# Optimization experiments

Measured on AMD Instinct MI355X. Metric: run time of the kernel, lower is better.

## Reference

```python
import jax, jax.numpy as jnp
from jax import lax
import numpy as np

N, C, D, KNN = 32768, 1000, 1024, 16
EPS_EUC = 1e-12
EPS_COS = 1e-8
COS_THRESH = 0.85


def setup_inputs() -> dict:
    key = jax.random.key(0)
    k1, k2, k3 = jax.random.split(key, 3)
    feature = jax.random.normal(k1, (N, D), dtype=jnp.float32)
    pred = jax.random.normal(k2, (N, C), dtype=jnp.float32)
    unlabeled_index = jnp.arange(N, dtype=jnp.int64) if jax.config.jax_enable_x64 else jnp.arange(N, dtype=jnp.int32)
    # module state: centroids (from FeaturePool), top-N score buffer (init -1), fake index buffer (init -1)
    centroids = jax.random.normal(k3, (C, D), dtype=jnp.float32)
    pred_top_N = jnp.full((C, KNN), -1.0, dtype=jnp.float32)
    fake_index = jnp.full((C, KNN), -1, dtype=jnp.int32)
    return {"feature": feature, "pred": pred, "unlabeled_index": unlabeled_index,
            "centroids": centroids, "pred_top_N": pred_top_N, "fake_index": fake_index}


def reference(feature, pred, unlabeled_index, centroids, pred_top_N, fake_index):
    xx = jnp.sum(feature * feature, axis=1, keepdims=True)          # [N,1]
    yy = jnp.sum(centroids * centroids, axis=1)[None, :]            # [1,C]
    euc = jnp.sqrt(jnp.clip(xx + yy - 2.0 * (feature @ centroids.T), EPS_EUC, None))
    euc_id = jnp.argmin(euc, axis=1)                                # [N]

    scores = jnp.max(jax.nn.softmax(pred, axis=1), axis=1)          # [N] max softmax prob

    # cosine similarity of every sample to every centroid [N, C]
    f_n = feature / jnp.clip(jnp.linalg.norm(feature, axis=1, keepdims=True), EPS_COS, None)
    c_n = centroids / jnp.clip(jnp.linalg.norm(centroids, axis=1, keepdims=True), EPS_COS, None)
    cos = f_n @ c_n.T
    label_idx = jnp.argmax(cos, axis=1)                             # [N]
    cos_max = jnp.max(cos, axis=1)                                  # [N]

    # label[i] = label_idx if (cos-argmax == euc-argmin and cos_max > 0.85) else -1
    label = jnp.where((label_idx == euc_id) & (cos_max > COS_THRESH),
                      label_idx.astype(jnp.float32), -1.0)

    # sequential bounded top-N scatter update of (pred_top_N, fake_index)
    def step(carry, x):
        ptn, fidx = carry
        li, sc, ui = x
        row = ptn[li]                        # [KNN]
        mi = jnp.argmin(row)
        upd = sc > row[mi]
        ptn = ptn.at[li, mi].set(jnp.where(upd, sc, row[mi]))
        fidx = fidx.at[li, mi].set(jnp.where(upd, ui.astype(fidx.dtype), fidx[li, mi]))
        return (ptn, fidx), None

    (ptn_new, fidx_new), _ = lax.scan(step, (pred_top_N, fake_index),
                                      (label_idx, scores, unlabeled_index))
    return label, ptn_new, fidx_new
```

## Files before the change

kernel.cpp:

```cpp
#include <hip/hip_runtime.h>
#include <hip/hip_bf16.h>
#include <math.h>

#define NS 32768
#define NC 1000
#define CP 1024
#define DD 1024
#define KN 16

typedef __attribute__((ext_vector_type(8))) short bf16x8;
typedef __attribute__((ext_vector_type(4))) float f32x4;
typedef __attribute__((ext_vector_type(4))) float float4v;
typedef __attribute__((ext_vector_type(4))) int int4v;
typedef __attribute__((ext_vector_type(8))) unsigned short u16x8;
typedef __attribute__((ext_vector_type(4))) unsigned short u16x4;

__device__ __forceinline__ unsigned short f2bf(float f) {
  unsigned u = __float_as_uint(f);
  u += 0x7FFFu + ((u >> 16) & 1u);
  return (unsigned short)(u >> 16);
}
__device__ __forceinline__ float bf2f(unsigned short h) {
  return __uint_as_float(((unsigned)h) << 16);
}

#define GLL16(g, l) __builtin_amdgcn_global_load_lds( \
    (const __attribute__((address_space(1))) void*)(g), \
    (__attribute__((address_space(3))) void*)(l), 16, 0, 0)

__global__ __launch_bounds__(256) void k_cast_cent(
    const float* __restrict__ Cm, unsigned short* __restrict__ Cb,
    float* __restrict__ cnorm2, float* __restrict__ invc) {
  int c = blockIdx.x;
  int tid = threadIdx.x;
  float sq = 0.f;
  if (c < NC) {
    float4v v = ((const float4v*)(Cm + (size_t)c * DD))[tid];
    sq = v[0]*v[0] + v[1]*v[1] + v[2]*v[2] + v[3]*v[3];
    u16x4 o = { f2bf(v[0]), f2bf(v[1]), f2bf(v[2]), f2bf(v[3]) };
    *(u16x4*)(Cb + (size_t)c * DD + tid * 4) = o;
  } else {
    u16x4 z = { 0, 0, 0, 0 };
    *(u16x4*)(Cb + (size_t)c * DD + tid * 4) = z;
  }
  for (int off = 32; off; off >>= 1) sq += __shfl_xor(sq, off);
  __shared__ float red[4];
  int lane = tid & 63, wid = tid >> 6;
  if (!lane) red[wid] = sq;
  __syncthreads();
  if (!tid) {
    float s = red[0] + red[1] + red[2] + red[3];
    cnorm2[c] = s;
    float n = sqrtf(s); if (n < 1e-8f) n = 1e-8f;
    invc[c] = (c < NC) ? 1.0f / n : 0.0f;
  }
}

__global__ __launch_bounds__(256) void k_cast_feat(
    const float* __restrict__ A, unsigned short* __restrict__ Ab) {
  int t = blockIdx.x * 256 + threadIdx.x;
  const float4v* src = (const float4v*)A + (size_t)t * 2;
  float4v a = src[0], b = src[1];
  u16x8 o = { f2bf(a[0]), f2bf(a[1]), f2bf(a[2]), f2bf(a[3]),
              f2bf(b[0]), f2bf(b[1]), f2bf(b[2]), f2bf(b[3]) };
  *(u16x8*)(Ab + (size_t)t * 8) = o;
}

#define MF(a_, b_, c_) __builtin_amdgcn_mfma_f32_16x16x32_bf16(a_, b_, c_, 0, 0, 0)
#define RD(base_, i_) (*(const bf16x8*)((base_) + (i_) * 1024 + aoff))
#define SA(s_, b_) do { \
    GLL16(pA0 + (s_) * 32, ldsB + (b_) * 16384 + dA0); \
    GLL16(pA1 + (s_) * 32, ldsB + (b_) * 16384 + dA1); } while (0)
#define SB(s_, b_) do { \
    GLL16(pB0 + (s_) * 32, ldsB + 65536 + (b_) * 16384 + dA0); \
    GLL16(pB1 + (s_) * 32, ldsB + 65536 + (b_) * 16384 + dA1); } while (0)
#define VM4 asm volatile("s_waitcnt vmcnt(4)" ::: "memory")
#define VM0 asm volatile("s_waitcnt vmcnt(0)" ::: "memory")
#define MFMA4x4(M0) do { \
    acc[M0+0][0] = MF(af0, bv0, acc[M0+0][0]); \
    acc[M0+0][1] = MF(af0, bv1, acc[M0+0][1]); \
    acc[M0+0][2] = MF(af0, bv2, acc[M0+0][2]); \
    acc[M0+0][3] = MF(af0, bv3, acc[M0+0][3]); \
    acc[M0+1][0] = MF(af1, bv0, acc[M0+1][0]); \
    acc[M0+1][1] = MF(af1, bv1, acc[M0+1][1]); \
    acc[M0+1][2] = MF(af1, bv2, acc[M0+1][2]); \
    acc[M0+1][3] = MF(af1, bv3, acc[M0+1][3]); \
    acc[M0+2][0] = MF(af2, bv0, acc[M0+2][0]); \
    acc[M0+2][1] = MF(af2, bv1, acc[M0+2][1]); \
    acc[M0+2][2] = MF(af2, bv2, acc[M0+2][2]); \
    acc[M0+2][3] = MF(af2, bv3, acc[M0+2][3]); \
    acc[M0+3][0] = MF(af3, bv0, acc[M0+3][0]); \
    acc[M0+3][1] = MF(af3, bv1, acc[M0+3][1]); \
    acc[M0+3][2] = MF(af3, bv2, acc[M0+3][2]); \
    acc[M0+3][3] = MF(af3, bv3, acc[M0+3][3]); } while (0)
#define GSTEP(s_, STAGEA_, STAGEB_, GATE_) do { \
    const char* Ab_ = ldsB + ((s_) & 3) * 16384 + wrOff; \
    const char* Bb_ = ldsB + 65536 + ((s_) & 3) * 16384 + wcOff; \
    af0 = RD(Ab_, 0); af1 = RD(Ab_, 1); af2 = RD(Ab_, 2); af3 = RD(Ab_, 3); \
    bv0 = RD(Bb_, 0); bv1 = RD(Bb_, 1); bv2 = RD(Bb_, 2); bv3 = RD(Bb_, 3); \
    STAGEA_; \
    __builtin_amdgcn_s_barrier(); \
    __builtin_amdgcn_s_setprio(1); \
    MFMA4x4(0); \
    __builtin_amdgcn_s_setprio(0); \
    __builtin_amdgcn_s_barrier(); \
    af0 = RD(Ab_, 4); af1 = RD(Ab_, 5); af2 = RD(Ab_, 6); af3 = RD(Ab_, 7); \
    STAGEB_; \
    __builtin_amdgcn_s_barrier(); \
    __builtin_amdgcn_s_setprio(1); \
    MFMA4x4(4); \
    __builtin_amdgcn_s_setprio(0); \
    GATE_; \
    __builtin_amdgcn_s_barrier(); \
  } while (0)

__global__ __launch_bounds__(512, 1) void k_gemm(
    const unsigned short* __restrict__ A,
    const unsigned short* __restrict__ B,
    unsigned short* __restrict__ Dout) {
  __shared__ unsigned short lds[65536];
  char* ldsB = (char*)lds;
  int tid = threadIdx.x, lane = tid & 63, wid = tid >> 6;
  int wr = wid >> 2, wc = wid & 3;
  int bid = (blockIdx.x & 7) * 64 + (blockIdx.x >> 3);
  int cb = bid & 3, rb = bid >> 2;
  int brow = rb * 256, bcol = cb * 256;

  f32x4 acc[8][4];
#pragma unroll
  for (int m = 0; m < 8; ++m)
#pragma unroll
    for (int n = 0; n < 4; ++n) acc[m][n] = (f32x4){0.f, 0.f, 0.f, 0.f};

  int f0 = wid * 64 + lane, f1 = f0 + 512;
  int gl0 = (f0 & 3) ^ ((f0 >> 3) & 3);
  int gl1 = (f1 & 3) ^ ((f1 >> 3) & 3);
  const unsigned short* pA0 = A + (size_t)(brow + (f0 >> 2)) * DD + gl0 * 8;
  const unsigned short* pA1 = A + (size_t)(brow + (f1 >> 2)) * DD + gl1 * 8;
  const unsigned short* pB0 = B + (size_t)(bcol + (f0 >> 2)) * DD + gl0 * 8;
  const unsigned short* pB1 = B + (size_t)(bcol + (f1 >> 2)) * DD + gl1 * 8;
  int dA0 = f0 * 16, dA1 = f1 * 16;

  int aoff = (lane & 15) * 64 + (((lane >> 4) ^ ((lane >> 1) & 3)) * 16);
  int wrOff = wr * 8192;
  int wcOff = wc * 4096;

  bf16x8 af0, af1, af2, af3, bv0, bv1, bv2, bv3;

  SA(0, 0); SB(0, 0);
  SA(1, 1); SB(1, 1);
  VM4;
  __builtin_amdgcn_s_barrier();

  for (int s = 0; s < 30; ++s) {
    int bn = (s & 3) ^ 2;
    GSTEP(s, SA(s + 2, bn), SB(s + 2, bn), VM4);
  }
  GSTEP(30, (void)0, (void)0, VM0);
  GSTEP(31, (void)0, (void)0, (void)0);

  int colb = bcol + wc * 64 + (lane & 15);
  int rowb = brow + wr * 128 + ((lane >> 4) << 2);
#pragma unroll
  for (int m = 0; m < 8; ++m)
#pragma unroll
    for (int n = 0; n < 4; ++n)
#pragma unroll
      for (int j = 0; j < 4; ++j)
        Dout[(size_t)(rowb + m * 16 + j) * CP + colb + n * 16] = f2bf(acc[m][n][j]);
}

__global__ __launch_bounds__(256) void k_score(
    const float* __restrict__ P, float* __restrict__ scores) {
  int i = blockIdx.x, tid = threadIdx.x;
  const float* row = P + (size_t)i * NC;
  bool act = tid < 250;
  float p0 = 0, p1 = 0, p2 = 0, p3 = 0, mx = -1e30f;
  if (act) {
    int b = tid * 4;
    p0 = row[b]; p1 = row[b + 1]; p2 = row[b + 2]; p3 = row[b + 3];
    mx = fmaxf(fmaxf(p0, p1), fmaxf(p2, p3));
  }
  for (int off = 32; off; off >>= 1) mx = fmaxf(mx, __shfl_xor(mx, off));
  __shared__ float wmax[4];
  __shared__ double wsum[4];
  int lane = tid & 63, wid = tid >> 6;
  if (!lane) wmax[wid] = mx;
  __syncthreads();
  float m = fmaxf(fmaxf(wmax[0], wmax[1]), fmaxf(wmax[2], wmax[3]));
  double s = 0.0;
  if (act)
    s = (double)__expf(p0 - m) + (double)__expf(p1 - m) +
        (double)__expf(p2 - m) + (double)__expf(p3 - m);
  for (int off = 32; off; off >>= 1) s += __shfl_xor(s, off);
  if (!lane) wsum[wid] = s;
  __syncthreads();
  if (!tid) scores[i] = (float)(1.0 / (wsum[0] + wsum[1] + wsum[2] + wsum[3]));
}

__global__ __launch_bounds__(256) void k_argmax(
    const unsigned short* __restrict__ Dot, const float* __restrict__ invc,
    const float* __restrict__ cnorm2, const float* __restrict__ feat,
    const float* __restrict__ cent, float* __restrict__ label_out,
    int* __restrict__ lidx) {
  __shared__ float s_inv[CP], s_cn[CP];
  int tid = threadIdx.x;
#pragma unroll
  for (int q = 0; q < 4; ++q) {
    int c = q * 256 + tid;
    s_inv[c] = invc[c]; s_cn[c] = cnorm2[c];
  }
  __syncthreads();
  int lane = tid & 63, wid = tid >> 6;
  int i = blockIdx.x * 4 + wid;
  const unsigned short* drow = Dot + (size_t)i * CP;

  float v[16];
  float dmax = -1e30f; int darg = CP;
  float emin = 1e30f;  int earg = CP;
#pragma unroll
  for (int it = 0; it < 16; ++it) {
    int c = it * 64 + lane;
    float val, ev;
    if (c < NC) {
      float d = bf2f(drow[c]);
      val = d * s_inv[c];
      ev = s_cn[c] - 2.0f * d;
    } else { val = -1e30f; ev = 1e30f; }
    v[it] = val;
    if (val > dmax) { dmax = val; darg = c; }
    if (ev < emin)  { emin = ev;  earg = c; }
  }
  for (int off = 32; off; off >>= 1) {
    float om = __shfl_xor(dmax, off); int oi = __shfl_xor(darg, off);
    if (om > dmax || (om == dmax && oi < darg)) { dmax = om; darg = oi; }
    float oe = __shfl_xor(emin, off); int oj = __shfl_xor(earg, off);
    if (oe < emin || (oe == emin && oj < earg)) { emin = oe; earg = oj; }
  }
  const float MARGIN = 0.15f;
  unsigned long long cmask[16]; int ccnt = 0;
#pragma unroll
  for (int it = 0; it < 16; ++it) {
    int c = it * 64 + lane;
    bool cand = (c < NC) && (v[it] >= dmax - MARGIN);
    cmask[it] = __ballot(cand);
    ccnt += __popcll(cmask[it]);
  }
  int finalArg = darg;
  double cosmax_d = -2.0;
  bool need = (ccnt > 1) || (dmax > 10.0f);
  if (need) {
    float xv[16]; double sx = 0.0;
    const float* xr = feat + (size_t)i * DD;
#pragma unroll
    for (int t = 0; t < 16; ++t) {
      float x = xr[t * 64 + lane]; xv[t] = x; sx += (double)x * (double)x;
    }
    for (int off = 32; off; off >>= 1) sx += __shfl_xor(sx, off);
    double nx = sqrt(sx); if (nx < 1e-8) nx = 1e-8;
    double best = -2.0; int besti = CP;
    for (int it = 0; it < 16; ++it) {
      unsigned long long mk = cmask[it];
      while (mk) {
        int b = __builtin_ctzll(mk); mk &= mk - 1;
        int c = it * 64 + b;
        const float* cr = cent + (size_t)c * DD;
        double s = 0.0, s2 = 0.0;
#pragma unroll
        for (int t = 0; t < 16; ++t) {
          double cv = (double)cr[t * 64 + lane];
          s += (double)xv[t] * cv; s2 += cv * cv;
        }
        for (int off = 32; off; off >>= 1) {
          s += __shfl_xor(s, off); s2 += __shfl_xor(s2, off);
        }
        double nc = sqrt(s2); if (nc < 1e-8) nc = 1e-8;
        double cs = s / (nx * nc);
        if (cs > best) { best = cs; besti = c; }
      }
    }
    finalArg = besti; cosmax_d = best;
  }
  if (!lane) {
    lidx[i] = finalArg;
    float lab = -1.0f;
    if (need && finalArg == earg && cosmax_d > 0.85) lab = (float)finalArg;
    label_out[i] = lab;
  }
}

__global__ __launch_bounds__(64) void k_scan(
    const int* __restrict__ lidx, const float* __restrict__ scores,
    const int* __restrict__ uidx, const float* __restrict__ ptn_in,
    const int* __restrict__ fidx_in, float* __restrict__ out_ptn,
    float* __restrict__ out_fidx) {
  int c = blockIdx.x;
  int lane = threadIdx.x;
  float row[KN]; int idx[KN];
#pragma unroll
  for (int j = 0; j < KN; ++j) {
    row[j] = ptn_in[c * KN + j];
    idx[j] = fidx_in[c * KN + j];
  }
  for (int base = 0; base < NS; base += 256) {
    int l0 = lidx[base + lane];
    int l1 = lidx[base + 64 + lane];
    int l2 = lidx[base + 128 + lane];
    int l3 = lidx[base + 192 + lane];
#pragma unroll
    for (int q = 0; q < 4; ++q) {
      int lab = (q == 0) ? l0 : (q == 1) ? l1 : (q == 2) ? l2 : l3;
      unsigned long long m = __ballot(lab == c);
      while (m) {
        int b = __builtin_ctzll(m); m &= m - 1;
        int i = base + q * 64 + b;
        float s = scores[i];
        int ui = uidx[i];
        int mi = 0; float mn = row[0];
#pragma unroll
        for (int t = 1; t < KN; ++t)
          if (row[t] < mn) { mn = row[t]; mi = t; }
        if (s > mn) {
#pragma unroll
          for (int t = 0; t < KN; ++t)
            if (t == mi) { row[t] = s; idx[t] = ui; }
        }
      }
    }
  }
  if (!lane) {
#pragma unroll
    for (int j = 0; j < KN; ++j) {
      out_ptn[c * KN + j] = row[j];
      out_fidx[c * KN + j] = (float)idx[j];
    }
  }
}

extern "C" void kernel_launch(void* const* d_in, const int* in_sizes, int n_in,
                              void* d_out, int out_size, void* d_ws, size_t ws_size,
                              hipStream_t stream) {
  const float* feature = (const float*)d_in[0];
  const float* pred    = (const float*)d_in[1];
  const int*   uidx    = (const int*)d_in[2];
  const float* cent    = (const float*)d_in[3];
  const float* ptn_in  = (const float*)d_in[4];
  const int*   fidx_in = (const int*)d_in[5];
  float* out = (float*)d_out;

  char* ws = (char*)d_ws;
  unsigned short* cent_bf = (unsigned short*)(ws);
  unsigned short* feat_bf = (unsigned short*)(ws + (2ull << 20));
  unsigned short* dot_bf  = (unsigned short*)(ws + (66ull << 20));
  float* scores = (float*)(ws + (130ull << 20));
  int*   lidx   = (int*)  (ws + (130ull << 20) + (128ull << 10));
  float* cnorm2 = (float*)(ws + (130ull << 20) + (256ull << 10));
  float* invc   = (float*)(ws + (130ull << 20) + (260ull << 10));

  hipLaunchKernelGGL(k_cast_cent, dim3(CP), dim3(256), 0, stream,
                     cent, cent_bf, cnorm2, invc);
  hipLaunchKernelGGL(k_cast_feat, dim3((NS * DD / 8) / 256), dim3(256), 0, stream,
                     feature, feat_bf);
  hipLaunchKernelGGL(k_gemm, dim3((NS / 256) * (CP / 256)), dim3(512), 0, stream,
                     feat_bf, cent_bf, dot_bf);
  hipLaunchKernelGGL(k_score, dim3(NS), dim3(256), 0, stream, pred, scores);
  hipLaunchKernelGGL(k_argmax, dim3(NS / 4), dim3(256), 0, stream,
                     dot_bf, invc, cnorm2, feature, cent, out, lidx);
  hipLaunchKernelGGL(k_scan, dim3(NC), dim3(64), 0, stream,
                     lidx, scores, uidx, ptn_in, fidx_in,
                     out + NS, out + NS + NC * KN);
}
```

Before: 237.6 us.

## Fuse feature fp32-to-bf16 cast into GEMM A-tile loading

Removes the separate feature cast kernel and has the GEMM load fp32 feature rows directly into registers, convert them to bf16 and write them to LDS. The pipeline is restructured with ping-pong register buffers for A, async global-to-LDS loads kept only for B, and fewer barriers per k-step. This drops a 128MB fp32 read plus a 64MB bf16 write/read round trip. In exchange the GEMM now reads fp32 A from global once per column block (4x redundancy), and adds register pressure and VALU conversion work inside the MFMA loop.

Result: no change. 242.2 us (+2.0%).

```diff
diff --git a/kernel.cpp b/kernel.cpp
--- a/kernel.cpp
+++ b/kernel.cpp
@@ -56,26 +56,31 @@
   }
 }
 
-__global__ __launch_bounds__(256) void k_cast_feat(
-    const float* __restrict__ A, unsigned short* __restrict__ Ab) {
-  int t = blockIdx.x * 256 + threadIdx.x;
-  const float4v* src = (const float4v*)A + (size_t)t * 2;
-  float4v a = src[0], b = src[1];
-  u16x8 o = { f2bf(a[0]), f2bf(a[1]), f2bf(a[2]), f2bf(a[3]),
-              f2bf(b[0]), f2bf(b[1]), f2bf(b[2]), f2bf(b[3]) };
-  *(u16x8*)(Ab + (size_t)t * 8) = o;
-}
-
 #define MF(a_, b_, c_) __builtin_amdgcn_mfma_f32_16x16x32_bf16(a_, b_, c_, 0, 0, 0)
 #define RD(base_, i_) (*(const bf16x8*)((base_) + (i_) * 1024 + aoff))
-#define SA(s_, b_) do { \
-    GLL16(pA0 + (s_) * 32, ldsB + (b_) * 16384 + dA0); \
-    GLL16(pA1 + (s_) * 32, ldsB + (b_) * 16384 + dA1); } while (0)
-#define SB(s_, b_) do { \
-    GLL16(pB0 + (s_) * 32, ldsB + 65536 + (b_) * 16384 + dA0); \
-    GLL16(pB1 + (s_) * 32, ldsB + 65536 + (b_) * 16384 + dA1); } while (0)
-#define VM4 asm volatile("s_waitcnt vmcnt(4)" ::: "memory")
+#define LAE(s_) do { \
+    ea = ((const float4v*)(pA0 + (s_) * 32))[0]; \
+    eb = ((const float4v*)(pA0 + (s_) * 32))[1]; \
+    ec = ((const float4v*)(pA1 + (s_) * 32))[0]; \
+    ed = ((const float4v*)(pA1 + (s_) * 32))[1]; } while (0)
+#define LAO(s_) do { \
+    oa = ((const float4v*)(pA0 + (s_) * 32))[0]; \
+    ob = ((const float4v*)(pA0 + (s_) * 32))[1]; \
+    oc = ((const float4v*)(pA1 + (s_) * 32))[0]; \
+    od = ((const float4v*)(pA1 + (s_) * 32))[1]; } while (0)
+#define SB2(s_) do { \
+    GLL16(pB0 + (s_) * 32, ldsB + 65536 + ((s_) & 3) * 16384 + dA0); \
+    GLL16(pB1 + (s_) * 32, ldsB + 65536 + ((s_) & 3) * 16384 + dA1); } while (0)
+#define CVW(s_, va, vb, vc, vd) do { \
+    u16x8 w0 = { f2bf(va[0]), f2bf(va[1]), f2bf(va[2]), f2bf(va[3]), \
+                 f2bf(vb[0]), f2bf(vb[1]), f2bf(vb[2]), f2bf(vb[3]) }; \
+    u16x8 w1 = { f2bf(vc[0]), f2bf(vc[1]), f2bf(vc[2]), f2bf(vc[3]), \
+                 f2bf(vd[0]), f2bf(vd[1]), f2bf(vd[2]), f2bf(vd[3]) }; \
+    *(u16x8*)(ldsB + ((s_) & 3) * 16384 + dA0) = w0; \
+    *(u16x8*)(ldsB + ((s_) & 3) * 16384 + dA1) = w1; } while (0)
+#define VM6 asm volatile("s_waitcnt vmcnt(6)" ::: "memory")
 #define VM0 asm volatile("s_waitcnt vmcnt(0)" ::: "memory")
+#define LGKM0 asm volatile("s_waitcnt lgkmcnt(0)" ::: "memory")
 #define MFMA4x4(M0) do { \
     acc[M0+0][0] = MF(af0, bv0, acc[M0+0][0]); \
     acc[M0+0][1] = MF(af0, bv1, acc[M0+0][1]); \
@@ -93,29 +98,23 @@
     acc[M0+3][1] = MF(af3, bv1, acc[M0+3][1]); \
     acc[M0+3][2] = MF(af3, bv2, acc[M0+3][2]); \
     acc[M0+3][3] = MF(af3, bv3, acc[M0+3][3]); } while (0)
-#define GSTEP(s_, STAGEA_, STAGEB_, GATE_) do { \
+#define KSTEP(s_, ISSUE_, WBANK_, GATE_) do { \
     const char* Ab_ = ldsB + ((s_) & 3) * 16384 + wrOff; \
     const char* Bb_ = ldsB + 65536 + ((s_) & 3) * 16384 + wcOff; \
     af0 = RD(Ab_, 0); af1 = RD(Ab_, 1); af2 = RD(Ab_, 2); af3 = RD(Ab_, 3); \
     bv0 = RD(Bb_, 0); bv1 = RD(Bb_, 1); bv2 = RD(Bb_, 2); bv3 = RD(Bb_, 3); \
-    STAGEA_; \
-    __builtin_amdgcn_s_barrier(); \
-    __builtin_amdgcn_s_setprio(1); \
-    MFMA4x4(0); \
-    __builtin_amdgcn_s_setprio(0); \
-    __builtin_amdgcn_s_barrier(); \
+    ISSUE_; \
+    __builtin_amdgcn_s_setprio(1); MFMA4x4(0); __builtin_amdgcn_s_setprio(0); \
     af0 = RD(Ab_, 4); af1 = RD(Ab_, 5); af2 = RD(Ab_, 6); af3 = RD(Ab_, 7); \
-    STAGEB_; \
-    __builtin_amdgcn_s_barrier(); \
-    __builtin_amdgcn_s_setprio(1); \
-    MFMA4x4(4); \
-    __builtin_amdgcn_s_setprio(0); \
+    WBANK_; \
+    __builtin_amdgcn_s_setprio(1); MFMA4x4(4); __builtin_amdgcn_s_setprio(0); \
+    LGKM0; \
     GATE_; \
     __builtin_amdgcn_s_barrier(); \
   } while (0)
 
 __global__ __launch_bounds__(512, 1) void k_gemm(
-    const unsigned short* __restrict__ A,
+    const float* __restrict__ Af,
     const unsigned short* __restrict__ B,
     unsigned short* __restrict__ Dout) {
   __shared__ unsigned short lds[65536];
@@ -135,8 +134,8 @@
   int f0 = wid * 64 + lane, f1 = f0 + 512;
   int gl0 = (f0 & 3) ^ ((f0 >> 3) & 3);
   int gl1 = (f1 & 3) ^ ((f1 >> 3) & 3);
-  const unsigned short* pA0 = A + (size_t)(brow + (f0 >> 2)) * DD + gl0 * 8;
-  const unsigned short* pA1 = A + (size_t)(brow + (f1 >> 2)) * DD + gl1 * 8;
+  const float* pA0 = Af + (size_t)(brow + (f0 >> 2)) * DD + gl0 * 8;
+  const float* pA1 = Af + (size_t)(brow + (f1 >> 2)) * DD + gl1 * 8;
   const unsigned short* pB0 = B + (size_t)(bcol + (f0 >> 2)) * DD + gl0 * 8;
   const unsigned short* pB1 = B + (size_t)(bcol + (f1 >> 2)) * DD + gl1 * 8;
   int dA0 = f0 * 16, dA1 = f1 * 16;
@@ -146,18 +145,21 @@
   int wcOff = wc * 4096;
 
   bf16x8 af0, af1, af2, af3, bv0, bv1, bv2, bv3;
-
-  SA(0, 0); SB(0, 0);
-  SA(1, 1); SB(1, 1);
-  VM4;
+  float4v ea, eb, ec, ed, oa, ob, oc, od;
+
+  LAE(0); SB2(0);
+  LAO(1); SB2(1);
+  CVW(0, ea, eb, ec, ed);
+  LGKM0;
+  VM6;
   __builtin_amdgcn_s_barrier();
 
-  for (int s = 0; s < 30; ++s) {
-    int bn = (s & 3) ^ 2;
-    GSTEP(s, SA(s + 2, bn), SB(s + 2, bn), VM4);
-  }
-  GSTEP(30, (void)0, (void)0, VM0);
-  GSTEP(31, (void)0, (void)0, (void)0);
+  for (int s = 0; s < 30; s += 2) {
+    KSTEP(s,     { LAE(s + 2); SB2(s + 2); }, CVW(s + 1, oa, ob, oc, od), VM6);
+    KSTEP(s + 1, { LAO(s + 3); SB2(s + 3); }, CVW(s + 2, ea, eb, ec, ed), VM6);
+  }
+  KSTEP(30, (void)0, CVW(31, oa, ob, oc, od), VM0);
+  KSTEP(31, (void)0, (void)0, (void)0);
 
   int colb = bcol + wc * 64 + (lane & 15);
   int rowb = brow + wr * 128 + ((lane >> 4) << 2);
@@ -350,7 +352,6 @@
 
   char* ws = (char*)d_ws;
   unsigned short* cent_bf = (unsigned short*)(ws);
-  unsigned short* feat_bf = (unsigned short*)(ws + (2ull << 20));
   unsigned short* dot_bf  = (unsigned short*)(ws + (66ull << 20));
   float* scores = (float*)(ws + (130ull << 20));
   int*   lidx   = (int*)  (ws + (130ull << 20) + (128ull << 10));
@@ -359,10 +360,8 @@
 
   hipLaunchKernelGGL(k_cast_cent, dim3(CP), dim3(256), 0, stream,
                      cent, cent_bf, cnorm2, invc);
-  hipLaunchKernelGGL(k_cast_feat, dim3((NS * DD / 8) / 256), dim3(256), 0, stream,
-                     feature, feat_bf);
   hipLaunchKernelGGL(k_gemm, dim3((NS / 256) * (CP / 256)), dim3(512), 0, stream,
-                     feat_bf, cent_bf, dot_bf);
+                     feature, cent_bf, dot_bf);
   hipLaunchKernelGGL(k_score, dim3(NS), dim3(256), 0, stream, pred, scores);
   hipLaunchKernelGGL(k_argmax, dim3(NS / 4), dim3(256), 0, stream,
                      dot_bf, invc, cnorm2, feature, cent, out, lidx);
```
